# Optimization experiments

Measured on AMD Instinct MI355X. Metric: run time of the kernel, lower is better.

## Reference

```python
import jax, jax.numpy as jnp
import numpy as np

N_NODES = 50000
N_EDGES = 400000
IN_DIM = 64
HID = 128
HEADS = 4
NEG_SLOPE = 0.2


def gat_conv(x, src, dst, W, a_src, a_dst, b, heads, out_ch, concat):
    N = x.shape[0]
    h = (x @ W).reshape(N, heads, out_ch)                 # [N,H,C]
    alpha_s = jnp.einsum('nhc,hc->nh', h, a_src)          # [N,H]
    alpha_d = jnp.einsum('nhc,hc->nh', h, a_dst)
    e = jax.nn.leaky_relu(alpha_s[src] + alpha_d[dst], NEG_SLOPE)  # [E,H]
    m = jax.ops.segment_max(e, dst, num_segments=N)
    m = jnp.where(jnp.isfinite(m), m, 0.0)
    ex = jnp.exp(e - m[dst])
    s = jax.ops.segment_sum(ex, dst, num_segments=N)
    alpha = ex / s[dst]                                   # segment softmax over incoming edges
    out = jax.ops.segment_sum(h[src] * alpha[:, :, None], dst, num_segments=N)  # [N,H,C]
    out = out.reshape(N, heads * out_ch) if concat else out.mean(axis=1)
    return out + b


def setup_inputs() -> dict:
    key = jax.random.key(0)
    ks = jax.random.split(key, 20)
    g = lambda i, shape, sc: (jax.random.normal(ks[i], shape, jnp.float32) * sc)
    x = g(0, (N_NODES, IN_DIM), 1.0)
    edge_index = jax.random.randint(ks[1], (2, N_EDGES), 0, N_NODES, dtype=jnp.int32)
    d = {
        'x': x, 'edge_index': edge_index,
        'W1': g(2, (IN_DIM, HEADS * HID), 0.1), 'a_src1': g(3, (HEADS, HID), 0.1), 'a_dst1': g(4, (HEADS, HID), 0.1), 'b1': jnp.zeros((HEADS * HID,), jnp.float32),
        'W2': g(5, (HEADS * HID, HEADS * HID), 0.05), 'a_src2': g(6, (HEADS, HID), 0.1), 'a_dst2': g(7, (HEADS, HID), 0.1), 'b2': jnp.zeros((HEADS * HID,), jnp.float32),
        'W3': g(8, (HEADS * HID, HID), 0.05), 'a_src3': g(9, (1, HID), 0.1), 'a_dst3': g(10, (1, HID), 0.1), 'b3': jnp.zeros((HID,), jnp.float32),
        'fc1_w': g(11, (HID, HID // 2), 0.1), 'fc1_b': jnp.zeros((HID // 2,), jnp.float32),
        'fc2_w': g(12, (HID // 2, 1), 0.1), 'fc2_b': jnp.zeros((1,), jnp.float32),
    }
    return d


def reference(x, edge_index, W1, a_src1, a_dst1, b1, W2, a_src2, a_dst2, b2, W3, a_src3, a_dst3, b3, fc1_w, fc1_b, fc2_w, fc2_b):
    N = x.shape[0]
    loop = jnp.arange(N, dtype=edge_index.dtype)
    src = jnp.concatenate([edge_index[0], loop])  # PyG GATConv adds self-loops by default
    dst = jnp.concatenate([edge_index[1], loop])
    h = jax.nn.elu(gat_conv(x, src, dst, W1, a_src1, a_dst1, b1, HEADS, HID, True))
    h = jax.nn.elu(gat_conv(h, src, dst, W2, a_src2, a_dst2, b2, HEADS, HID, True))
    h = jax.nn.elu(gat_conv(h, src, dst, W3, a_src3, a_dst3, b3, 1, HID, False))
    h = jax.nn.relu(h @ fc1_w + fc1_b)
    return jax.nn.sigmoid(h @ fc2_w + fc2_b)  # [N, 1]
```

## Files before the change

kernel.cpp:

```cpp
#include <hip/hip_runtime.h>
#include <math.h>

typedef __attribute__((ext_vector_type(8))) short short8;
typedef __attribute__((ext_vector_type(4))) float f32x4;
typedef unsigned short u16;
typedef unsigned int u32;

__device__ inline u16 f2b(float f) {
  u32 u = __float_as_uint(f);
  return (u16)((u + 0x7FFFu + ((u >> 16) & 1u)) >> 16);
}
__device__ inline float b2f(u16 b) { return __uint_as_float((u32)b << 16); }
__device__ inline float lrelu(float v) { return v > 0.f ? v : 0.2f * v; }
__device__ inline float elu1(float v) { return v > 0.f ? v : __expf(v) - 1.f; }

__device__ inline void gld_lds16(const void* g, void* l) {
  __builtin_amdgcn_global_load_lds((const __attribute__((address_space(1))) void*)g,
                                   (__attribute__((address_space(3))) void*)l, 16, 0, 0);
}

__global__ void fused_prep(const float* __restrict__ W1, u16* __restrict__ Wt1,
                           const float* __restrict__ W2, u16* __restrict__ Wt2,
                           const float* __restrict__ W3, u16* __restrict__ Wt3,
                           const int* __restrict__ ei, int E0, int ET,
                           int* __restrict__ deg, const float* __restrict__ as1,
                           const float* __restrict__ ad1, float* __restrict__ wsd) {
  int i = blockIdx.x * blockDim.x + threadIdx.x;
  if (i < 64 * 512) {
    int n = i >> 6, k = i & 63;
    Wt1[n * 64 + k] = f2b(W1[k * 512 + n]);
    return;
  }
  i -= 64 * 512;
  if (i < 512 * 512) {
    int n = i >> 9, k = i & 511;
    Wt2[n * 512 + k] = f2b(W2[k * 512 + n]);
    return;
  }
  i -= 512 * 512;
  if (i < 512 * 128) {
    int n = i >> 9, k = i & 511;
    Wt3[n * 512 + k] = f2b(W3[k * 128 + n]);
    return;
  }
  i -= 512 * 128;
  if (i < ET) {
    int d = (i < E0) ? ei[E0 + i] : (i - E0);
    atomicAdd(&deg[d], 1);
    return;
  }
  i -= ET;
  if (i < 512) {
    int k = i >> 3, c8 = i & 7, hh = c8 & 3;
    const float* a = (c8 >= 4) ? ad1 : as1;
    float s = 0.f;
    for (int c = 0; c < 128; ++c) s += W1[k * 512 + hh * 128 + c] * a[hh * 128 + c];
    wsd[k * 8 + c8] = s;
  }
}

__global__ __launch_bounds__(256) void gemm_bf16_gat(
    const u16* __restrict__ A, const u16* __restrict__ Bt, u16* __restrict__ Hb,
    const float* __restrict__ a_src, const float* __restrict__ a_dst,
    float* __restrict__ aS, float* __restrict__ aD, int M, int HC, int K, int Hh,
    int gy, int nStrips) {
  int mIdx, nIdx;
  if (nStrips == 4) {
    int l = blockIdx.x;
    int xcd = l & 7, k = l >> 3;
    nIdx = k & 3;
    mIdx = xcd + 8 * (k >> 2);
    if (mIdx >= gy) return;
  } else {
    mIdx = blockIdx.x;
    nIdx = 0;
  }
  __shared__ u16 As[2][128 * 32];
  __shared__ u16 Bs[2][128 * 32];
  __shared__ float sRed[2][2][128];
  const int tid = threadIdx.x;
  const int w = tid >> 6, lane = tid & 63;
  const int wm = w >> 1, wn = w & 1;
  const int q = lane >> 4, l15 = lane & 15;
  const int nBase = nIdx * 128;
  const int mBase = mIdx * 128;
  const int h = nBase >> 7;
  const int srow = lane >> 2;
  const int ssw = ((lane & 3) ^ ((lane >> 3) & 3)) * 8;
  const int rq = (q ^ ((l15 >> 1) & 3)) * 8;

  f32x4 acc[4][4];
#pragma unroll
  for (int i = 0; i < 4; ++i)
#pragma unroll
    for (int j = 0; j < 4; ++j) acc[i][j] = (f32x4){0.f, 0.f, 0.f, 0.f};

  const int nSteps = K >> 5;
#pragma unroll
  for (int r = 0; r < 2; ++r) {
    int lrow0 = w * 32 + r * 16;
    int ga = mBase + lrow0 + srow;
    if (ga >= M) ga = M - 1;
    gld_lds16(A + (size_t)ga * K + ssw, &As[0][lrow0 * 32]);
    int gb = nBase + lrow0 + srow;
    gld_lds16(Bt + (size_t)gb * K + ssw, &Bs[0][lrow0 * 32]);
  }
  __syncthreads();
  int cur = 0;
  for (int step = 0; step < nSteps; ++step) {
    const int k0n = (step + 1) << 5;
    if (k0n < K) {
#pragma unroll
      for (int r = 0; r < 2; ++r) {
        int lrow0 = w * 32 + r * 16;
        int ga = mBase + lrow0 + srow;
        if (ga >= M) ga = M - 1;
        gld_lds16(A + (size_t)ga * K + k0n + ssw, &As[cur ^ 1][lrow0 * 32]);
        int gb = nBase + lrow0 + srow;
        gld_lds16(Bt + (size_t)gb * K + k0n + ssw, &Bs[cur ^ 1][lrow0 * 32]);
      }
    }
    short8 af[4], bf[4];
#pragma unroll
    for (int i = 0; i < 4; ++i)
      af[i] = *(const short8*)&As[cur][(wm * 64 + i * 16 + l15) * 32 + rq];
#pragma unroll
    for (int j = 0; j < 4; ++j)
      bf[j] = *(const short8*)&Bs[cur][(wn * 64 + j * 16 + l15) * 32 + rq];
#pragma unroll
    for (int i = 0; i < 4; ++i)
#pragma unroll
      for (int j = 0; j < 4; ++j)
        acc[i][j] = __builtin_amdgcn_mfma_f32_16x16x32_bf16(af[i], bf[j], acc[i][j], 0, 0, 0);
    __syncthreads();
    cur ^= 1;
  }

  float asv[4], adv[4];
#pragma unroll
  for (int j = 0; j < 4; ++j) {
    int cw = wn * 64 + j * 16 + l15;
    asv[j] = a_src[h * 128 + cw];
    adv[j] = a_dst[h * 128 + cw];
  }
#pragma unroll
  for (int mi = 0; mi < 4; ++mi) {
#pragma unroll
    for (int r = 0; r < 4; ++r) {
      int row = mBase + wm * 64 + mi * 16 + q * 4 + r;
      float s = 0.f, d = 0.f;
#pragma unroll
      for (int j = 0; j < 4; ++j) {
        float v = acc[mi][j][r];
        s = fmaf(v, asv[j], s);
        d = fmaf(v, adv[j], d);
        if (row < M) Hb[(size_t)row * HC + nBase + wn * 64 + j * 16 + l15] = f2b(v);
      }
#pragma unroll
      for (int o = 8; o; o >>= 1) {
        s += __shfl_xor(s, o);
        d += __shfl_xor(d, o);
      }
      if (l15 == 0) {
        int lr = wm * 64 + mi * 16 + q * 4 + r;
        sRed[0][wn][lr] = s;
        sRed[1][wn][lr] = d;
      }
    }
  }
  __syncthreads();
  if (tid < 128) {
    int row = mBase + tid;
    if (row < M) {
      aS[(size_t)row * Hh + h] = sRed[0][0][tid] + sRed[0][1][tid];
      aD[(size_t)row * Hh + h] = sRed[1][0][tid] + sRed[1][1][tid];
    }
  }
}

__global__ __launch_bounds__(256) void gemm_bf16_l3(
    const u16* __restrict__ A, const u16* __restrict__ Bt,
    const float* __restrict__ a_src, const float* __restrict__ a_dst,
    u16* __restrict__ Hb, float* __restrict__ aS, float* __restrict__ aD, int M) {
  __shared__ u16 As[2][64 * 32];
  __shared__ u16 Bs[2][128 * 32];
  const int tid = threadIdx.x;
  const int w = tid >> 6, lane = tid & 63;
  const int q = lane >> 4, l15 = lane & 15;
  const int mBase = blockIdx.x * 64;
  const int ssw = ((lane & 3) ^ ((lane >> 3) & 3)) * 8;
  const int rq = (q ^ ((l15 >> 1) & 3)) * 8;
  const int arow = w * 16 + (lane >> 2);

  f32x4 acc[8];
#pragma unroll
  for (int j = 0; j < 8; ++j) acc[j] = (f32x4){0.f, 0.f, 0.f, 0.f};

  {
    int ga = mBase + arow;
    if (ga >= M) ga = M - 1;
    gld_lds16(A + (size_t)ga * 512 + ssw, &As[0][w * 512]);
#pragma unroll
    for (int r = 0; r < 2; ++r) {
      int brow = r * 64 + w * 16 + (lane >> 2);
      gld_lds16(Bt + (size_t)brow * 512 + ssw, &Bs[0][(r * 64 + w * 16) * 32]);
    }
  }
  __syncthreads();
  int cur = 0;
  for (int step = 0; step < 16; ++step) {
    if (step < 15) {
      const int k0n = (step + 1) << 5;
      int ga = mBase + arow;
      if (ga >= M) ga = M - 1;
      gld_lds16(A + (size_t)ga * 512 + k0n + ssw, &As[cur ^ 1][w * 512]);
#pragma unroll
      for (int r = 0; r < 2; ++r) {
        int brow = r * 64 + w * 16 + (lane >> 2);
        gld_lds16(Bt + (size_t)brow * 512 + k0n + ssw,
                  &Bs[cur ^ 1][(r * 64 + w * 16) * 32]);
      }
    }
    short8 af = *(const short8*)&As[cur][(w * 16 + l15) * 32 + rq];
    short8 bf[8];
#pragma unroll
    for (int j = 0; j < 8; ++j)
      bf[j] = *(const short8*)&Bs[cur][(j * 16 + l15) * 32 + rq];
#pragma unroll
    for (int j = 0; j < 8; ++j)
      acc[j] = __builtin_amdgcn_mfma_f32_16x16x32_bf16(af, bf[j], acc[j], 0, 0, 0);
    __syncthreads();
    cur ^= 1;
  }

  float asv[8], adv[8];
#pragma unroll
  for (int j = 0; j < 8; ++j) {
    asv[j] = a_src[j * 16 + l15];
    adv[j] = a_dst[j * 16 + l15];
  }
#pragma unroll
  for (int r = 0; r < 4; ++r) {
    int row = mBase + w * 16 + q * 4 + r;
    float s = 0.f, d = 0.f;
#pragma unroll
    for (int j = 0; j < 8; ++j) {
      float v = acc[j][r];
      s = fmaf(v, asv[j], s);
      d = fmaf(v, adv[j], d);
      if (row < M) Hb[(size_t)row * 128 + j * 16 + l15] = f2b(v);
    }
#pragma unroll
    for (int o = 8; o; o >>= 1) {
      s += __shfl_xor(s, o);
      d += __shfl_xor(d, o);
    }
    if (l15 == 0 && row < M) {
      aS[row] = s;
      aD[row] = d;
    }
  }
}

__global__ __launch_bounds__(256) void gemm_bd_l1(
    const u16* __restrict__ A, const u16* __restrict__ Bt,
    const float* __restrict__ bias, u16* __restrict__ outB, int M, int gy) {
  int l = blockIdx.x;
  int xcd = l & 7, kk = l >> 3;
  int nIdx = kk & 3;
  int mIdx = xcd + 8 * (kk >> 2);
  if (mIdx >= gy) return;
  __shared__ u16 As[2][128 * 32];
  __shared__ u16 Bs[2][128 * 32];
  const int tid = threadIdx.x;
  const int w = tid >> 6, lane = tid & 63;
  const int wm = w >> 1, wn = w & 1;
  const int q = lane >> 4, l15 = lane & 15;
  const int nBase = nIdx * 128, mBase = mIdx * 128;
  const int srow = lane >> 2;
  const int ssw = ((lane & 3) ^ ((lane >> 3) & 3)) * 8;
  const int rq = (q ^ ((l15 >> 1) & 3)) * 8;

  f32x4 acc[4][4];
#pragma unroll
  for (int i = 0; i < 4; ++i)
#pragma unroll
    for (int j = 0; j < 4; ++j) acc[i][j] = (f32x4){0.f, 0.f, 0.f, 0.f};

#pragma unroll
  for (int r = 0; r < 2; ++r) {
    int lrow0 = w * 32 + r * 16;
    int ga = mBase + lrow0 + srow;
    if (ga >= M) ga = M - 1;
    gld_lds16(A + (size_t)ga * 256 + nIdx * 64 + ssw, &As[0][lrow0 * 32]);
    int gb = nBase + lrow0 + srow;
    gld_lds16(Bt + (size_t)gb * 64 + ssw, &Bs[0][lrow0 * 32]);
  }
  __syncthreads();
  int cur = 0;
#pragma unroll
  for (int step = 0; step < 2; ++step) {
    if (step == 0) {
#pragma unroll
      for (int r = 0; r < 2; ++r) {
        int lrow0 = w * 32 + r * 16;
        int ga = mBase + lrow0 + srow;
        if (ga >= M) ga = M - 1;
        gld_lds16(A + (size_t)ga * 256 + nIdx * 64 + 32 + ssw, &As[1][lrow0 * 32]);
        int gb = nBase + lrow0 + srow;
        gld_lds16(Bt + (size_t)gb * 64 + 32 + ssw, &Bs[1][lrow0 * 32]);
      }
    }
    short8 af[4], bf[4];
#pragma unroll
    for (int i = 0; i < 4; ++i)
      af[i] = *(const short8*)&As[cur][(wm * 64 + i * 16 + l15) * 32 + rq];
#pragma unroll
    for (int j = 0; j < 4; ++j)
      bf[j] = *(const short8*)&Bs[cur][(wn * 64 + j * 16 + l15) * 32 + rq];
#pragma unroll
    for (int i = 0; i < 4; ++i)
#pragma unroll
      for (int j = 0; j < 4; ++j)
        acc[i][j] = __builtin_amdgcn_mfma_f32_16x16x32_bf16(af[i], bf[j], acc[i][j], 0, 0, 0);
    __syncthreads();
    cur ^= 1;
  }

  float bvv[4];
#pragma unroll
  for (int j = 0; j < 4; ++j) bvv[j] = bias[nBase + wn * 64 + j * 16 + l15];
#pragma unroll
  for (int mi = 0; mi < 4; ++mi)
#pragma unroll
    for (int r = 0; r < 4; ++r) {
      int row = mBase + wm * 64 + mi * 16 + q * 4 + r;
      if (row < M) {
#pragma unroll
        for (int j = 0; j < 4; ++j) {
          float v = elu1(acc[mi][j][r] + bvv[j]);
          outB[(size_t)row * 512 + nBase + wn * 64 + j * 16 + l15] = f2b(v);
        }
      }
    }
}

__global__ __launch_bounds__(256) void scan_chunk(const int* __restrict__ deg,
                                                  int* __restrict__ incl,
                                                  int* __restrict__ bsums, int N) {
  __shared__ int sdata[256];
  const int t = threadIdx.x;
  const int base = blockIdx.x * 2048;
  int v[8];
  int sum = 0;
#pragma unroll
  for (int i = 0; i < 8; ++i) {
    int idx = base + t * 8 + i;
    v[i] = (idx < N) ? deg[idx] : 0;
    sum += v[i];
  }
  sdata[t] = sum;
  __syncthreads();
  for (int off = 1; off < 256; off <<= 1) {
    int x = (t >= off) ? sdata[t - off] : 0;
    __syncthreads();
    sdata[t] += x;
    __syncthreads();
  }
  int run = (t > 0) ? sdata[t - 1] : 0;
#pragma unroll
  for (int i = 0; i < 8; ++i) {
    int idx = base + t * 8 + i;
    run += v[i];
    if (idx < N) incl[idx] = run;
  }
  if (t == 255) bsums[blockIdx.x] = sdata[255];
}

__global__ void scan_final(const int* __restrict__ incl, const int* __restrict__ bsums,
                           int* __restrict__ rowptr, int N, int nb) {
  int i = blockIdx.x * blockDim.x + threadIdx.x;
  if (i >= N) return;
  int chunk = i >> 11;
  int pre = 0;
  for (int j = 0; j < chunk; ++j) pre += bsums[j];
  rowptr[i + 1] = incl[i] + pre;
  if (i == 0) rowptr[0] = 0;
}

__global__ void csr_fill(const int* __restrict__ ei, int E0, int ET,
                         const int* __restrict__ rowptr, int* __restrict__ cnt,
                         int* __restrict__ csr_src, int* __restrict__ csr_dst,
                         const float* __restrict__ aS, const float* __restrict__ aD,
                         float* __restrict__ elog) {
  int e = blockIdx.x * blockDim.x + threadIdx.x;
  if (e >= ET) return;
  int s, d;
  if (e < E0) { s = ei[e]; d = ei[E0 + e]; }
  else        { s = e - E0; d = e - E0; }
  int pos = atomicAdd(&cnt[d], 1);
  int slot = rowptr[d] + pos;
  csr_src[slot] = s;
  csr_dst[slot] = d;
  float4 a = *(const float4*)&aS[(size_t)s * 4];
  float4 b = *(const float4*)&aD[(size_t)d * 4];
  float4 r;
  r.x = lrelu(a.x + b.x);
  r.y = lrelu(a.y + b.y);
  r.z = lrelu(a.z + b.z);
  r.w = lrelu(a.w + b.w);
  *(float4*)&elog[(size_t)slot * 4] = r;
}

__global__ __launch_bounds__(256) void asad_x(const float* __restrict__ xf,
                                              const float* __restrict__ wsd,
                                              float* __restrict__ aS,
                                              float* __restrict__ aD, int N) {
  const int wid = (int)((blockIdx.x * (blockDim.x >> 6)) + (threadIdx.x >> 6));
  const int lane = threadIdx.x & 63;
  if (wid >= N) return;
  float xv = xf[(size_t)wid * 64 + lane];
  float4 w0 = *(const float4*)&wsd[lane * 8];
  float4 w1 = *(const float4*)&wsd[lane * 8 + 4];
  float s[8] = {xv * w0.x, xv * w0.y, xv * w0.z, xv * w0.w,
                xv * w1.x, xv * w1.y, xv * w1.z, xv * w1.w};
#pragma unroll
  for (int i = 0; i < 8; ++i)
#pragma unroll
    for (int o = 32; o; o >>= 1) s[i] += __shfl_xor(s[i], o);
  if (lane == 0) {
    *(float4*)&aS[(size_t)wid * 4] = make_float4(s[0], s[1], s[2], s[3]);
    *(float4*)&aD[(size_t)wid * 4] = make_float4(s[4], s[5], s[6], s[7]);
  }
}

__global__ __launch_bounds__(256) void edge_logits(const int* __restrict__ csr_src,
                                                   const int* __restrict__ csr_dst,
                                                   const float* __restrict__ aS,
                                                   const float* __restrict__ aD,
                                                   float* __restrict__ elog, int ET,
                                                   int Hh) {
  int e = blockIdx.x * blockDim.x + threadIdx.x;
  if (e >= ET) return;
  int s = csr_src[e], d = csr_dst[e];
  if (Hh == 4) {
    float4 a = *(const float4*)&aS[(size_t)s * 4];
    float4 b = *(const float4*)&aD[(size_t)d * 4];
    float4 r;
    r.x = lrelu(a.x + b.x);
    r.y = lrelu(a.y + b.y);
    r.z = lrelu(a.z + b.z);
    r.w = lrelu(a.w + b.w);
    *(float4*)&elog[(size_t)e * 4] = r;
  } else {
    elog[e] = lrelu(aS[s] + aD[d]);
  }
}

__global__ __launch_bounds__(256) void gat_agg_x(
    const int* __restrict__ rowptr, const int* __restrict__ csr_src,
    const float* __restrict__ xf, const float* __restrict__ elog,
    u16* __restrict__ aggB, int N) {
  const int wid = (int)((blockIdx.x * (blockDim.x >> 6)) + (threadIdx.x >> 6));
  const int lane = threadIdx.x & 63;
  if (wid >= N) return;
  const int beg = rowptr[wid];
  const int deg = rowptr[wid + 1] - beg;
  const int h = lane >> 4;
  const int e16 = lane & 15;
  float acc[4] = {};

  if (deg <= 16) {
    int srcv = 0;
    float l = -1e30f;
    if (e16 < deg) {
      srcv = csr_src[beg + e16];
      l = elog[(size_t)(beg + e16) * 4 + h];
    }
    float xv[16];
#pragma unroll
    for (int j = 0; j < 16; ++j)
      if (j < deg) {
        int s = __shfl(srcv, j);
        xv[j] = xf[(size_t)s * 64 + lane];
      }
    float m = l;
#pragma unroll
    for (int o = 8; o; o >>= 1) m = fmaxf(m, __shfl_xor(m, o));
    float pexp = (e16 < deg) ? __expf(l - m) : 0.f;
    float cs = pexp;
#pragma unroll
    for (int o = 8; o; o >>= 1) cs += __shfl_xor(cs, o);
    pexp *= (1.f / cs);
#pragma unroll
    for (int j = 0; j < 16; ++j)
      if (j < deg) {
        float w0 = __shfl(pexp, j);
        float w1 = __shfl(pexp, 16 | j);
        float w2 = __shfl(pexp, 32 | j);
        float w3 = __shfl(pexp, 48 | j);
        acc[0] = fmaf(w0, xv[j], acc[0]);
        acc[1] = fmaf(w1, xv[j], acc[1]);
        acc[2] = fmaf(w2, xv[j], acc[2]);
        acc[3] = fmaf(w3, xv[j], acc[3]);
      }
  } else {
    float m = -1e30f, ssum = 0.f;
    for (int c = 0; c < deg; c += 16) {
      const int ce = min(16, deg - c);
      int srcv = 0;
      float l = -1e30f;
      if (e16 < ce) {
        srcv = csr_src[beg + c + e16];
        l = elog[(size_t)(beg + c + e16) * 4 + h];
      }
      float xv[16];
#pragma unroll
      for (int j = 0; j < 16; ++j)
        if (j < ce) {
          int s = __shfl(srcv, j);
          xv[j] = xf[(size_t)s * 64 + lane];
        }
      float cm = l;
#pragma unroll
      for (int o = 8; o; o >>= 1) cm = fmaxf(cm, __shfl_xor(cm, o));
      float pexp, cs;
      if (c == 0) {
        m = cm;
        pexp = (e16 < ce) ? __expf(l - m) : 0.f;
        cs = pexp;
#pragma unroll
        for (int o = 8; o; o >>= 1) cs += __shfl_xor(cs, o);
        ssum = cs;
      } else {
        float newm = fmaxf(m, cm);
        float r = __expf(m - newm);
        m = newm;
        pexp = (e16 < ce) ? __expf(l - m) : 0.f;
        cs = pexp;
#pragma unroll
        for (int o = 8; o; o >>= 1) cs += __shfl_xor(cs, o);
        ssum = ssum * r + cs;
#pragma unroll
        for (int i = 0; i < 4; ++i) acc[i] *= r;
      }
#pragma unroll
      for (int j = 0; j < 16; ++j)
        if (j < ce) {
          float w0 = __shfl(pexp, j);
          float w1 = __shfl(pexp, 16 | j);
          float w2 = __shfl(pexp, 32 | j);
          float w3 = __shfl(pexp, 48 | j);
          acc[0] = fmaf(w0, xv[j], acc[0]);
          acc[1] = fmaf(w1, xv[j], acc[1]);
          acc[2] = fmaf(w2, xv[j], acc[2]);
          acc[3] = fmaf(w3, xv[j], acc[3]);
        }
    }
    const float inv = 1.f / ssum;
#pragma unroll
    for (int i = 0; i < 4; ++i) acc[i] *= inv;
  }
#pragma unroll
  for (int hh = 0; hh < 4; ++hh)
    aggB[((size_t)wid * 4 + hh) * 64 + lane] = f2b(acc[hh]);
}

#define ACC8(A, pv, wgt)                                             \
  A[0] = fmaf(wgt, __uint_as_float(pv.x << 16), A[0]);               \
  A[1] = fmaf(wgt, __uint_as_float(pv.x & 0xffff0000u), A[1]);       \
  A[2] = fmaf(wgt, __uint_as_float(pv.y << 16), A[2]);               \
  A[3] = fmaf(wgt, __uint_as_float(pv.y & 0xffff0000u), A[3]);       \
  A[4] = fmaf(wgt, __uint_as_float(pv.z << 16), A[4]);               \
  A[5] = fmaf(wgt, __uint_as_float(pv.z & 0xffff0000u), A[5]);       \
  A[6] = fmaf(wgt, __uint_as_float(pv.w << 16), A[6]);               \
  A[7] = fmaf(wgt, __uint_as_float(pv.w & 0xffff0000u), A[7]);

__global__ __launch_bounds__(256) void gat_fused_agg(
    const int* __restrict__ rowptr, const int* __restrict__ csr_src,
    const u16* __restrict__ Hb, const float* __restrict__ elog,
    const float* __restrict__ bias, u16* __restrict__ outB, int N) {
  const int wid = (int)((blockIdx.x * (blockDim.x >> 6)) + (threadIdx.x >> 6));
  const int lane = threadIdx.x & 63;
  if (wid >= N) return;
  const int beg = rowptr[wid];
  const int deg = rowptr[wid + 1] - beg;

  const int h = lane >> 4;
  const int e16 = lane & 15;
  const int c0 = lane * 8;
  const int hbase = lane & 48;
  float acc[8] = {};

  if (deg <= 16) {
    int srcv = 0;
    float l = -1e30f;
    if (e16 < deg) {
      srcv = csr_src[beg + e16];
      l = elog[(size_t)(beg + e16) * 4 + h];
    }
    uint4 pC[4];
#pragma unroll
    for (int j = 0; j < 4; ++j)
      if (j < deg) {
        int s = __shfl(srcv, j);
        pC[j] = *(const uint4*)&Hb[(size_t)s * 512 + c0];
      }
    float m = l;
#pragma unroll
    for (int o = 8; o; o >>= 1) m = fmaxf(m, __shfl_xor(m, o));
    float pexp = (e16 < deg) ? __expf(l - m) : 0.f;
    float cs = pexp;
#pragma unroll
    for (int o = 8; o; o >>= 1) cs += __shfl_xor(cs, o);
    pexp *= (1.f / cs);
    int e = 0;
    for (; e + 4 < deg; e += 4) {
      uint4 pN[4];
      int rem = deg - e - 4;
#pragma unroll
      for (int j = 0; j < 4; ++j)
        if (j < rem) {
          int s = __shfl(srcv, e + 4 + j);
          pN[j] = *(const uint4*)&Hb[(size_t)s * 512 + c0];
        }
#pragma unroll
      for (int j = 0; j < 4; ++j) {
        float wgt = __shfl(pexp, hbase | (e + j));
        ACC8(acc, pC[j], wgt)
      }
#pragma unroll
      for (int j = 0; j < 4; ++j) pC[j] = pN[j];
    }
#pragma unroll
    for (int j = 0; j < 4; ++j)
      if (j < deg - e) {
        float wgt = __shfl(pexp, hbase | (e + j));
        ACC8(acc, pC[j], wgt)
      }
  } else {
    float m = -1e30f, ssum = 0.f;
    for (int c = 0; c < deg; c += 16) {
      const int ce = min(16, deg - c);
      int srcv = 0;
      float l = -1e30f;
      if (e16 < ce) {
        srcv = csr_src[beg + c + e16];
        l = elog[(size_t)(beg + c + e16) * 4 + h];
      }
      float cm = l;
#pragma unroll
      for (int o = 8; o; o >>= 1) cm = fmaxf(cm, __shfl_xor(cm, o));
      float pexp, cs;
      if (c == 0) {
        m = cm;
        pexp = __expf(l - m);
        cs = pexp;
#pragma unroll
        for (int o = 8; o; o >>= 1) cs += __shfl_xor(cs, o);
        ssum = cs;
      } else {
        float newm = fmaxf(m, cm);
        float r = __expf(m - newm);
        m = newm;
        pexp = __expf(l - m);
        cs = pexp;
#pragma unroll
        for (int o = 8; o; o >>= 1) cs += __shfl_xor(cs, o);
        ssum = ssum * r + cs;
#pragma unroll
        for (int i = 0; i < 8; ++i) acc[i] *= r;
      }
      int e = 0;
      for (; e + 4 <= ce; e += 4) {
        int se0 = __shfl(srcv, e + 0), se1 = __shfl(srcv, e + 1);
        int se2 = __shfl(srcv, e + 2), se3 = __shfl(srcv, e + 3);
        float w0 = __shfl(pexp, hbase | (e + 0)), w1 = __shfl(pexp, hbase | (e + 1));
        float w2 = __shfl(pexp, hbase | (e + 2)), w3 = __shfl(pexp, hbase | (e + 3));
        uint4 p0 = *(const uint4*)&Hb[(size_t)se0 * 512 + c0];
        uint4 p1 = *(const uint4*)&Hb[(size_t)se1 * 512 + c0];
        uint4 p2 = *(const uint4*)&Hb[(size_t)se2 * 512 + c0];
        uint4 p3 = *(const uint4*)&Hb[(size_t)se3 * 512 + c0];
        ACC8(acc, p0, w0)
        ACC8(acc, p1, w1)
        ACC8(acc, p2, w2)
        ACC8(acc, p3, w3)
      }
      for (; e < ce; ++e) {
        int se = __shfl(srcv, e);
        float wgt = __shfl(pexp, hbase | e);
        uint4 pv = *(const uint4*)&Hb[(size_t)se * 512 + c0];
        ACC8(acc, pv, wgt)
      }
    }
    const float inv = 1.f / ssum;
#pragma unroll
    for (int i = 0; i < 8; ++i) acc[i] *= inv;
  }

  float bv[8];
  *(float4*)&bv[0] = *(const float4*)&bias[c0];
  *(float4*)&bv[4] = *(const float4*)&bias[c0 + 4];
  u16 packed[8];
#pragma unroll
  for (int i = 0; i < 8; ++i) {
    float v = elu1(acc[i] + bv[i]);
    packed[i] = f2b(v);
  }
  *(uint4*)&outB[(size_t)wid * 512 + c0] = *(const uint4*)packed;
}

__global__ __launch_bounds__(256) void gat_agg_h1(
    const int* __restrict__ rowptr, const int* __restrict__ csr_src,
    const u16* __restrict__ Hb, const float* __restrict__ elog,
    const float* __restrict__ bias, float* __restrict__ outF, int N) {
  const int wid = (int)((blockIdx.x * (blockDim.x >> 6)) + (threadIdx.x >> 6));
  const int lane = threadIdx.x & 63;
  if (wid >= N) return;
  const int beg = rowptr[wid];
  const int deg = rowptr[wid + 1] - beg;
  const int g = lane & 15;
  const int es = lane >> 4;
  const int c0 = g * 8;
  float acc[8] = {};

  if (deg <= 64) {
    int srcv = 0;
    float l = -1e30f;
    if (lane < deg) {
      srcv = csr_src[beg + lane];
      l = elog[beg + lane];
    }
    const int dm1 = deg - 1;
    uint4 pC;
    {
      int s = __shfl(srcv, min(es, dm1));
      pC = *(const uint4*)&Hb[(size_t)s * 128 + c0];
    }
    float m = l;
#pragma unroll
    for (int o = 32; o; o >>= 1) m = fmaxf(m, __shfl_xor(m, o));
    float pexp = (lane < deg) ? __expf(l - m) : 0.f;
    float cs = pexp;
#pragma unroll
    for (int o = 32; o; o >>= 1) cs += __shfl_xor(cs, o);
    pexp *= (1.f / cs);
    int t = 0;
    for (; t + 4 < deg; t += 4) {
      uint4 pN;
      {
        int s = __shfl(srcv, min(t + 4 + es, dm1));
        pN = *(const uint4*)&Hb[(size_t)s * 128 + c0];
      }
      float w = __shfl(pexp, t + es);
      ACC8(acc, pC, w)
      pC = pN;
    }
    {
      int idx = t + es;
      float w = __shfl(pexp, min(idx, dm1));
      if (idx > dm1) w = 0.f;
      ACC8(acc, pC, w)
    }
  } else {
    float m = -1e30f, ssum = 0.f;
    for (int c = 0; c < deg; c += 64) {
      const int ce = min(64, deg - c);
      int srcv = 0;
      float l = -1e30f;
      if (lane < ce) {
        srcv = csr_src[beg + c + lane];
        l = elog[beg + c + lane];
      }
      float cm = l;
#pragma unroll
      for (int o = 32; o; o >>= 1) cm = fmaxf(cm, __shfl_xor(cm, o));
      float pexp, cs;
      if (c == 0) {
        m = cm;
        pexp = __expf(l - m);
        cs = pexp;
#pragma unroll
        for (int o = 32; o; o >>= 1) cs += __shfl_xor(cs, o);
        ssum = cs;
      } else {
        float newm = fmaxf(m, cm);
        float r = __expf(m - newm);
        m = newm;
        pexp = __expf(l - m);
        cs = pexp;
#pragma unroll
        for (int o = 32; o; o >>= 1) cs += __shfl_xor(cs, o);
        ssum = ssum * r + cs;
#pragma unroll
        for (int i = 0; i < 8; ++i) acc[i] *= r;
      }
      for (int t = 0; t < ce; t += 4) {
        int idx = t + es;
        int se = __shfl(srcv, idx & 63);
        float wgt = __shfl(pexp, idx & 63);
        if (idx < ce) {
          uint4 pv = *(const uint4*)&Hb[(size_t)se * 128 + c0];
          ACC8(acc, pv, wgt)
        }
      }
    }
    const float inv = 1.f / ssum;
#pragma unroll
    for (int i = 0; i < 8; ++i) acc[i] *= inv;
  }
#pragma unroll
  for (int i = 0; i < 8; ++i) {
    acc[i] += __shfl_xor(acc[i], 16);
    acc[i] += __shfl_xor(acc[i], 32);
  }
  if (lane < 16) {
    float o[8];
#pragma unroll
    for (int i = 0; i < 8; ++i) o[i] = elu1(acc[i] + bias[c0 + i]);
    *(float4*)&outF[(size_t)wid * 128 + c0] = make_float4(o[0], o[1], o[2], o[3]);
    *(float4*)&outF[(size_t)wid * 128 + c0 + 4] = make_float4(o[4], o[5], o[6], o[7]);
  }
}

__global__ __launch_bounds__(256) void fc_head(const float* __restrict__ A,
                                               const float* __restrict__ B,
                                               const float* __restrict__ bias,
                                               const float* __restrict__ w2,
                                               const float* __restrict__ b2,
                                               float* __restrict__ out, int M) {
  __shared__ float As[16][64];
  __shared__ float Bs[16][64];
  __shared__ float sP[64][17];
  const int tid = threadIdx.x;
  const int tx = tid & 15, ty = tid >> 4;
  const int mBase = blockIdx.y * 64;
  const int aRow = tid >> 2;
  const int aK = (tid & 3) << 2;
  const int bC = tid & 63;
  const int bR0 = tid >> 6;
  const int K = 128, N = 64;
  float acc[4][4] = {};
  for (int k0 = 0; k0 < K; k0 += 16) {
    float4 av = make_float4(0.f, 0.f, 0.f, 0.f);
    int gr = mBase + aRow;
    if (gr < M) av = *(const float4*)&A[(size_t)gr * K + k0 + aK];
    As[aK + 0][aRow] = av.x;
    As[aK + 1][aRow] = av.y;
    As[aK + 2][aRow] = av.z;
    As[aK + 3][aRow] = av.w;
#pragma unroll
    for (int i = 0; i < 4; ++i) {
      int r = bR0 + i * 4;
      Bs[r][bC] = B[(size_t)(k0 + r) * N + bC];
    }
    __syncthreads();
#pragma unroll
    for (int k = 0; k < 16; ++k) {
      float4 a = *(const float4*)&As[k][ty * 4];
      float4 b = *(const float4*)&Bs[k][tx * 4];
      float ar[4] = {a.x, a.y, a.z, a.w};
      float br[4] = {b.x, b.y, b.z, b.w};
#pragma unroll
      for (int i = 0; i < 4; ++i)
#pragma unroll
        for (int j = 0; j < 4; ++j) acc[i][j] = fmaf(ar[i], br[j], acc[i][j]);
    }
    __syncthreads();
  }
  float4 bv = *(const float4*)&bias[tx * 4];
  float4 wv = *(const float4*)&w2[tx * 4];
#pragma unroll
  for (int i = 0; i < 4; ++i) {
    float p = 0.f;
    p = fmaf(fmaxf(acc[i][0] + bv.x, 0.f), wv.x, p);
    p = fmaf(fmaxf(acc[i][1] + bv.y, 0.f), wv.y, p);
    p = fmaf(fmaxf(acc[i][2] + bv.z, 0.f), wv.z, p);
    p = fmaf(fmaxf(acc[i][3] + bv.w, 0.f), wv.w, p);
    sP[ty * 4 + i][tx] = p;
  }
  __syncthreads();
  if (tid < 64) {
    int row = mBase + tid;
    if (row < M) {
      float s = 0.f;
#pragma unroll
      for (int t = 0; t < 16; ++t) s += sP[tid][t];
      out[row] = 1.f / (1.f + expf(-(s + b2[0])));
    }
  }
}

extern "C" void kernel_launch(void* const* d_in, const int* in_sizes, int n_in,
                              void* d_out, int out_size, void* d_ws, size_t ws_size,
                              hipStream_t stream) {
  const float* x    = (const float*)d_in[0];
  const int*   ei   = (const int*)d_in[1];
  const float* W1   = (const float*)d_in[2];
  const float* as1  = (const float*)d_in[3];
  const float* ad1  = (const float*)d_in[4];
  const float* b1   = (const float*)d_in[5];
  const float* W2   = (const float*)d_in[6];
  const float* as2  = (const float*)d_in[7];
  const float* ad2  = (const float*)d_in[8];
  const float* b2   = (const float*)d_in[9];
  const float* W3   = (const float*)d_in[10];
  const float* as3  = (const float*)d_in[11];
  const float* ad3  = (const float*)d_in[12];
  const float* b3   = (const float*)d_in[13];
  const float* fc1w = (const float*)d_in[14];
  const float* fc1b = (const float*)d_in[15];
  const float* fc2w = (const float*)d_in[16];
  const float* fc2b = (const float*)d_in[17];
  float* out = (float*)d_out;

  const int N  = in_sizes[0] / 64;
  const int E0 = in_sizes[1] / 2;
  const int ET = E0 + N;

  char* ws = (char*)d_ws;
  size_t off = 0;
  auto alloc = [&](size_t bytes) -> void* {
    void* p = ws + off;
    off += (bytes + 255) & ~(size_t)255;
    return p;
  };
  u16*   bufXb   = (u16*)alloc((size_t)N * 512 * 2);
  u16*   bufHb   = (u16*)alloc((size_t)N * 512 * 2);
  float* bufF    = (float*)alloc((size_t)N * 128 * 4);
  float* aS      = (float*)alloc((size_t)N * 4 * 4);
  float* aD      = (float*)alloc((size_t)N * 4 * 4);
  u16*   Wt1     = (u16*)alloc((size_t)512 * 64 * 2);
  u16*   Wt2     = (u16*)alloc((size_t)512 * 512 * 2);
  u16*   Wt3     = (u16*)alloc((size_t)128 * 512 * 2);
  u16*   aggB    = (u16*)alloc((size_t)N * 256 * 2);
  float* wsd     = (float*)alloc((size_t)64 * 8 * 4);
  int*   degcnt  = (int*)alloc((size_t)2 * N * 4);
  int*   deg     = degcnt;
  int*   cnt     = degcnt + N;
  int*   incl    = (int*)alloc((size_t)N * 4);
  int*   rowptr  = (int*)alloc((size_t)(N + 1) * 4);
  int*   bsums   = (int*)alloc(256 * 4);
  int*   csr_src = (int*)alloc((size_t)ET * 4);
  int*   csr_dst = (int*)alloc((size_t)ET * 4);
  float* elog    = (float*)alloc((size_t)ET * 4 * 4);
  (void)ws_size; (void)n_in; (void)out_size;

  hipMemsetAsync(degcnt, 0, (size_t)2 * N * 4, stream);
  const int prepTotal = 64 * 512 + 512 * 512 + 512 * 128 + ET + 512;
  hipLaunchKernelGGL(fused_prep, dim3((prepTotal + 255) / 256), dim3(256), 0, stream,
                     W1, Wt1, W2, Wt2, W3, Wt3, ei, E0, ET, deg, as1, ad1, wsd);

  int nb = (N + 2047) / 2048;
  hipLaunchKernelGGL(scan_chunk, dim3(nb), dim3(256), 0, stream, deg, incl, bsums, N);
  hipLaunchKernelGGL(scan_final, dim3((N + 255) / 256), dim3(256), 0, stream, incl, bsums,
                     rowptr, N, nb);

  const int gy = (N + 127) / 128;
  const int grid4 = ((gy + 7) / 8) * 8 * 4;
  const int aggGrid = (N + 3) / 4;
  int eb = (ET + 255) / 256;

  hipLaunchKernelGGL(asad_x, dim3(aggGrid), dim3(256), 0, stream, x, wsd, aS, aD, N);
  hipLaunchKernelGGL(csr_fill, dim3(eb), dim3(256), 0, stream, ei, E0, ET, rowptr, cnt,
                     csr_src, csr_dst, aS, aD, elog);
  hipLaunchKernelGGL(gat_agg_x, dim3(aggGrid), dim3(256), 0, stream, rowptr, csr_src, x,
                     elog, aggB, N);
  hipLaunchKernelGGL(gemm_bd_l1, dim3(grid4), dim3(256), 0, stream, aggB, Wt1, b1,
                     bufXb, N, gy);

  hipLaunchKernelGGL(gemm_bf16_gat, dim3(grid4), dim3(256), 0, stream, bufXb, Wt2, bufHb,
                     as2, ad2, aS, aD, N, 512, 512, 4, gy, 4);
  hipLaunchKernelGGL(edge_logits, dim3(eb), dim3(256), 0, stream, csr_src, csr_dst, aS,
                     aD, elog, ET, 4);
  hipLaunchKernelGGL(gat_fused_agg, dim3(aggGrid), dim3(256), 0, stream, rowptr,
                     csr_src, bufHb, elog, b2, bufXb, N);

  hipLaunchKernelGGL(gemm_bf16_l3, dim3((N + 63) / 64), dim3(256), 0, stream, bufXb,
                     Wt3, as3, ad3, bufHb, aS, aD, N);
  hipLaunchKernelGGL(edge_logits, dim3(eb), dim3(256), 0, stream, csr_src, csr_dst, aS,
                     aD, elog, ET, 1);
  hipLaunchKernelGGL(gat_agg_h1, dim3(aggGrid), dim3(256), 0, stream, rowptr, csr_src,
                     bufHb, elog, b3, bufF, N);

  hipLaunchKernelGGL(fc_head, dim3(1, (N + 63) / 64), dim3(256), 0, stream, bufF, fc1w,
                     fc1b, fc2w, fc2b, out, N);
}
```

Baseline: 440.7 us.

## Fuse layer-3 edge logits and MLP head into final aggregation kernel

The separate edge_logits pass for layer 3 is removed; the layer-3 aggregation now computes leaky-relu logits inline from per-node alpha_src/alpha_dst. The fc1/relu/fc2/sigmoid head is also computed per node inside the aggregation wavefront using shuffles, so the fp32 hidden buffer and the fc_head kernel go away. This saves two launches and the write and re-read of the edge logit array and the N×128 float buffer. In exchange each wave does 128 serial shuffle-FMA steps and reads fc1 weights per node (likely cache-resident).

```diff
diff --git a/kernel.cpp b/kernel.cpp
--- a/kernel.cpp
+++ b/kernel.cpp
@@ -712,8 +712,11 @@
 
 __global__ __launch_bounds__(256) void gat_agg_h1(
     const int* __restrict__ rowptr, const int* __restrict__ csr_src,
-    const u16* __restrict__ Hb, const float* __restrict__ elog,
-    const float* __restrict__ bias, float* __restrict__ outF, int N) {
+    const u16* __restrict__ Hb, const float* __restrict__ aSb,
+    const float* __restrict__ aDb, const float* __restrict__ bias,
+    const float* __restrict__ fc1w, const float* __restrict__ fc1b,
+    const float* __restrict__ fc2w, const float* __restrict__ fc2b,
+    float* __restrict__ out, int N) {
   const int wid = (int)((blockIdx.x * (blockDim.x >> 6)) + (threadIdx.x >> 6));
   const int lane = threadIdx.x & 63;
   if (wid >= N) return;
@@ -722,21 +725,20 @@
   const int g = lane & 15;
   const int es = lane >> 4;
   const int c0 = g * 8;
+  const float adh = aDb[wid];
   float acc[8] = {};
 
   if (deg <= 64) {
     int srcv = 0;
-    float l = -1e30f;
-    if (lane < deg) {
-      srcv = csr_src[beg + lane];
-      l = elog[beg + lane];
-    }
+    if (lane < deg) srcv = csr_src[beg + lane];
+    float av = aSb[srcv];
     const int dm1 = deg - 1;
     uint4 pC;
     {
       int s = __shfl(srcv, min(es, dm1));
       pC = *(const uint4*)&Hb[(size_t)s * 128 + c0];
     }
+    float l = (lane < deg) ? lrelu(av + adh) : -1e30f;
     float m = l;
 #pragma unroll
     for (int o = 32; o; o >>= 1) m = fmaxf(m, __shfl_xor(m, o));
@@ -770,7 +772,7 @@
       float l = -1e30f;
       if (lane < ce) {
         srcv = csr_src[beg + c + lane];
-        l = elog[beg + c + lane];
+        l = lrelu(aSb[srcv] + adh);
       }
       float cm = l;
 #pragma unroll
@@ -814,81 +816,27 @@
     acc[i] += __shfl_xor(acc[i], 16);
     acc[i] += __shfl_xor(acc[i], 32);
   }
-  if (lane < 16) {
-    float o[8];
-#pragma unroll
-    for (int i = 0; i < 8; ++i) o[i] = elu1(acc[i] + bias[c0 + i]);
-    *(float4*)&outF[(size_t)wid * 128 + c0] = make_float4(o[0], o[1], o[2], o[3]);
-    *(float4*)&outF[(size_t)wid * 128 + c0 + 4] = make_float4(o[4], o[5], o[6], o[7]);
-  }
-}
-
-__global__ __launch_bounds__(256) void fc_head(const float* __restrict__ A,
-                                               const float* __restrict__ B,
-                                               const float* __restrict__ bias,
-                                               const float* __restrict__ w2,
-                                               const float* __restrict__ b2,
-                                               float* __restrict__ out, int M) {
-  __shared__ float As[16][64];
-  __shared__ float Bs[16][64];
-  __shared__ float sP[64][17];
-  const int tid = threadIdx.x;
-  const int tx = tid & 15, ty = tid >> 4;
-  const int mBase = blockIdx.y * 64;
-  const int aRow = tid >> 2;
-  const int aK = (tid & 3) << 2;
-  const int bC = tid & 63;
-  const int bR0 = tid >> 6;
-  const int K = 128, N = 64;
-  float acc[4][4] = {};
-  for (int k0 = 0; k0 < K; k0 += 16) {
-    float4 av = make_float4(0.f, 0.f, 0.f, 0.f);
-    int gr = mBase + aRow;
-    if (gr < M) av = *(const float4*)&A[(size_t)gr * K + k0 + aK];
-    As[aK + 0][aRow] = av.x;
-    As[aK + 1][aRow] = av.y;
-    As[aK + 2][aRow] = av.z;
-    As[aK + 3][aRow] = av.w;
-#pragma unroll
-    for (int i = 0; i < 4; ++i) {
-      int r = bR0 + i * 4;
-      Bs[r][bC] = B[(size_t)(k0 + r) * N + bC];
-    }
-    __syncthreads();
-#pragma unroll
-    for (int k = 0; k < 16; ++k) {
-      float4 a = *(const float4*)&As[k][ty * 4];
-      float4 b = *(const float4*)&Bs[k][tx * 4];
-      float ar[4] = {a.x, a.y, a.z, a.w};
-      float br[4] = {b.x, b.y, b.z, b.w};
-#pragma unroll
-      for (int i = 0; i < 4; ++i)
-#pragma unroll
-        for (int j = 0; j < 4; ++j) acc[i][j] = fmaf(ar[i], br[j], acc[i][j]);
-    }
-    __syncthreads();
-  }
-  float4 bv = *(const float4*)&bias[tx * 4];
-  float4 wv = *(const float4*)&w2[tx * 4];
-#pragma unroll
-  for (int i = 0; i < 4; ++i) {
-    float p = 0.f;
-    p = fmaf(fmaxf(acc[i][0] + bv.x, 0.f), wv.x, p);
-    p = fmaf(fmaxf(acc[i][1] + bv.y, 0.f), wv.y, p);
-    p = fmaf(fmaxf(acc[i][2] + bv.z, 0.f), wv.z, p);
-    p = fmaf(fmaxf(acc[i][3] + bv.w, 0.f), wv.w, p);
-    sP[ty * 4 + i][tx] = p;
-  }
-  __syncthreads();
-  if (tid < 64) {
-    int row = mBase + tid;
-    if (row < M) {
-      float s = 0.f;
-#pragma unroll
-      for (int t = 0; t < 16; ++t) s += sP[tid][t];
-      out[row] = 1.f / (1.f + expf(-(s + b2[0])));
-    }
-  }
+  float o[8];
+#pragma unroll
+  for (int i = 0; i < 8; ++i) o[i] = elu1(acc[i] + bias[c0 + i]);
+  float p0 = 0.f, p1 = 0.f, p2 = 0.f, p3 = 0.f;
+#pragma unroll
+  for (int k = 0; k < 128; k += 4) {
+    float v0 = __shfl(o[(k + 0) & 7], (k + 0) >> 3);
+    float v1 = __shfl(o[(k + 1) & 7], (k + 1) >> 3);
+    float v2 = __shfl(o[(k + 2) & 7], (k + 2) >> 3);
+    float v3 = __shfl(o[(k + 3) & 7], (k + 3) >> 3);
+    p0 = fmaf(v0, fc1w[(k + 0) * 64 + lane], p0);
+    p1 = fmaf(v1, fc1w[(k + 1) * 64 + lane], p1);
+    p2 = fmaf(v2, fc1w[(k + 2) * 64 + lane], p2);
+    p3 = fmaf(v3, fc1w[(k + 3) * 64 + lane], p3);
+  }
+  float p = (p0 + p1) + (p2 + p3);
+  p = fmaxf(p + fc1b[lane], 0.f);
+  float s = p * fc2w[lane];
+#pragma unroll
+  for (int off = 32; off; off >>= 1) s += __shfl_xor(s, off);
+  if (lane == 0) out[wid] = 1.f / (1.f + __expf(-(s + fc2b[0])));
 }
 
 extern "C" void kernel_launch(void* const* d_in, const int* in_sizes, int n_in,
@@ -927,7 +875,6 @@
   };
   u16*   bufXb   = (u16*)alloc((size_t)N * 512 * 2);
   u16*   bufHb   = (u16*)alloc((size_t)N * 512 * 2);
-  float* bufF    = (float*)alloc((size_t)N * 128 * 4);
   float* aS      = (float*)alloc((size_t)N * 4 * 4);
   float* aD      = (float*)alloc((size_t)N * 4 * 4);
   u16*   Wt1     = (u16*)alloc((size_t)512 * 64 * 2);
@@ -978,11 +925,6 @@
 
   hipLaunchKernelGGL(gemm_bf16_l3, dim3((N + 63) / 64), dim3(256), 0, stream, bufXb,
                      Wt3, as3, ad3, bufHb, aS, aD, N);
-  hipLaunchKernelGGL(edge_logits, dim3(eb), dim3(256), 0, stream, csr_src, csr_dst, aS,
-                     aD, elog, ET, 1);
   hipLaunchKernelGGL(gat_agg_h1, dim3(aggGrid), dim3(256), 0, stream, rowptr, csr_src,
-                     bufHb, elog, b3, bufF, N);
-
-  hipLaunchKernelGGL(fc_head, dim3(1, (N + 63) / 64), dim3(256), 0, stream, bufF, fc1w,
-                     fc1b, fc2w, fc2b, out, N);
-}
+                     bufHb, aS, aD, b3, fc1w, fc1b, fc2w, fc2b, out, N);
+}
```

Measured after the change: 485.0 us. 1.1x slower.
